# Kernel optimization log

Hardware: AMD Instinct MI355X
Metric: run time of the kernel (lower is better)

Reference implementation:

```python
import jax, jax.numpy as jnp
import numpy as np

B, P, L = 1024, 8, 16384  # batch, PRECISION_BITS, TRNG_BITSTREAM_LENGTH


def setup_inputs() -> dict:
    key = jax.random.key(0)
    k1, k2 = jax.random.split(key)
    num = jax.random.randint(k1, (B,), 0, 2 ** P, dtype=jnp.int32)
    # per-module TRNG bitstreams, length P + L (as in Module.__init__)
    r = jax.random.randint(k2, (B, P, P + L), 0, 2, dtype=jnp.int32)
    return {"num": num, "r": r}


def reference(num, r):
    # Module index i reads x[P-1-i] of the MSB-first binary string -> bit i (LSB-first)
    Bsz, Pb, T = r.shape
    Lb = T - Pb
    x = ((num[:, None] >> jnp.arange(Pb, dtype=num.dtype)) & 1).astype(r.dtype)  # [B,P]
    rt = jnp.moveaxis(r, -1, 0)  # [T,B,P]

    def step(y, r_c):
        # majority scheme: y_o = x&y | x&r | y&r  (vectorized over batch and modules)
        y_o = (x & y) | (x & r_c) | (y & r_c)
        # pipeline: y_i[i, t+1] = y_o[i-1, t]; module 0 keeps y_i = 0 forever
        y_next = jnp.concatenate([jnp.zeros((Bsz, 1), r.dtype), y_o[:, :-1]], axis=1)
        return y_next, y_o[:, -1]  # snarf last module's output

    _, outs = jax.lax.scan(step, jnp.zeros((Bsz, Pb), r.dtype), rt)  # outs: [T,B]
    # sn[cyc] = y_o[P-1] from cycle cyc-1; first P entries are invalid and trimmed
    sn = outs[Pb - 1 : Pb - 1 + Lb].T  # [B, L]
    return sn
```

## Files before the change

### kernel.cpp

```cpp
#include <hip/hip_runtime.h>


#define BATCH 1024
#define PBITS 8
#define LBITS 16384
#define TLEN (PBITS + LBITS)

typedef int v4i __attribute__((ext_vector_type(4)));

__global__ __launch_bounds__(256) void sng_kernel(const int* __restrict__ num,
                                                  const int* __restrict__ r,
                                                  int* __restrict__ out) {
    const int b = blockIdx.x >> 4;
    const int j = ((blockIdx.x & 15) << 8) | threadIdx.x;
    const int l = j << 2;

    const int nb = num[b];
    const int* rb = r + (size_t)b * (PBITS * TLEN) + l;

    v4i rv[PBITS];
#pragma unroll
    for (int i = 0; i < PBITS; ++i)
        rv[i] = __builtin_nontemporal_load(
            reinterpret_cast<const v4i*>(rb + i * (TLEN + 1)));

    v4i v = {0, 0, 0, 0};
#pragma unroll
    for (int i = 0; i < PBITS; ++i) {
        const int x = (nb >> i) & 1;
        const v4i xm = {-x, -x, -x, -x};
        v = (xm & (v | rv[i])) | (v & rv[i]);
    }

    const int tid = (b << 12) | j;
    __builtin_nontemporal_store(v, reinterpret_cast<v4i*>(out) + tid);
}

extern "C" void kernel_launch(void* const* d_in, const int* in_sizes, int n_in,
                              void* d_out, int out_size, void* d_ws, size_t ws_size,
                              hipStream_t stream) {
    const int* num = (const int*)d_in[0];
    const int* r   = (const int*)d_in[1];
    int* out = (int*)d_out;

    const int blocks = BATCH * (LBITS / 1024);
    sng_kernel<<<blocks, 256, 0, stream>>>(num, r, out);
}
```

Baseline: 670.4 us.

## Stage misaligned per-module rows through LDS with global_load_lds and bit-conditional updates

The kernel now copies each module's input row into shared memory with direct global-to-LDS loads using aligned 16-byte transfers, then reads it back at the per-module offset. Before, each row was read with unaligned vector loads because the stride is TLEN+1. It also replaces the masked majority with an OR or AND chosen by the bit of num, and gives each block 4096 outputs instead of 1024. The cost is two barriers per module, serialising load and compute with no double buffering, and fewer blocks overall.

```diff
diff --git a/kernel.cpp b/kernel.cpp
--- a/kernel.cpp
+++ b/kernel.cpp
@@ -6,34 +6,57 @@
 #define LBITS 16384
 #define TLEN (PBITS + LBITS)
 
-typedef int v4i __attribute__((ext_vector_type(4)));
+#define CHUNK 4096
+#define STAGE_DW 4104
+
+typedef const __attribute__((address_space(1))) void gvoid;
+typedef __attribute__((address_space(3))) void lvoid;
 
 __global__ __launch_bounds__(256) void sng_kernel(const int* __restrict__ num,
                                                   const int* __restrict__ r,
                                                   int* __restrict__ out) {
-    const int b = blockIdx.x >> 4;
-    const int j = ((blockIdx.x & 15) << 8) | threadIdx.x;
-    const int l = j << 2;
+    __shared__ int lds[STAGE_DW];
+
+    const int t = threadIdx.x;
+    const int b = blockIdx.x >> 2;
+    const int jb = (blockIdx.x & 3) << 12;
 
     const int nb = num[b];
-    const int* rb = r + (size_t)b * (PBITS * TLEN) + l;
+    const int* rowbase = r + (size_t)b * (PBITS * TLEN) + jb;
 
-    v4i rv[PBITS];
+    int v[16];
 #pragma unroll
-    for (int i = 0; i < PBITS; ++i)
-        rv[i] = __builtin_nontemporal_load(
-            reinterpret_cast<const v4i*>(rb + i * (TLEN + 1)));
+    for (int k = 0; k < 16; ++k) v[k] = 0;
 
-    v4i v = {0, 0, 0, 0};
 #pragma unroll
     for (int i = 0; i < PBITS; ++i) {
-        const int x = (nb >> i) & 1;
-        const v4i xm = {-x, -x, -x, -x};
-        v = (xm & (v | rv[i])) | (v & rv[i]);
+        const int* src = rowbase + i * TLEN;
+#pragma unroll
+        for (int k = 0; k < 4; ++k)
+            __builtin_amdgcn_global_load_lds((gvoid*)(src + 4 * (t + 256 * k)),
+                                             (lvoid*)(&lds[4 * (t + 256 * k)]),
+                                             16, 0, 0);
+        if (t < 2)
+            __builtin_amdgcn_global_load_lds((gvoid*)(src + 4 * (1024 + t)),
+                                             (lvoid*)(&lds[4 * (1024 + t)]),
+                                             16, 0, 0);
+        __syncthreads();
+
+        const int* lp = &lds[t + i];
+        if ((nb >> i) & 1) {
+#pragma unroll
+            for (int k = 0; k < 16; ++k) v[k] |= lp[256 * k];
+        } else {
+#pragma unroll
+            for (int k = 0; k < 16; ++k) v[k] &= lp[256 * k];
+        }
+        __syncthreads();
     }
 
-    const int tid = (b << 12) | j;
-    __builtin_nontemporal_store(v, reinterpret_cast<v4i*>(out) + tid);
+    int* ob = out + (size_t)b * LBITS + jb + t;
+#pragma unroll
+    for (int k = 0; k < 16; ++k)
+        __builtin_nontemporal_store(v[k], ob + 256 * k);
 }
 
 extern "C" void kernel_launch(void* const* d_in, const int* in_sizes, int n_in,
@@ -43,6 +66,6 @@
     const int* r   = (const int*)d_in[1];
     int* out = (int*)d_out;
 
-    const int blocks = BATCH * (LBITS / 1024);
+    const int blocks = BATCH * 4;
     sng_kernel<<<blocks, 256, 0, stream>>>(num, r, out);
 }
```

Result: slower. 699.2 us (+4.3%).
